# Kernel tuning notes

Hardware: AMD Instinct MI355X
Metric: run time of the kernel (lower is better)

## Reference

```python
import jax, jax.numpy as jnp
import numpy as np

NEG_INF = -1e30  # stand-in for float('-inf') that is fp16/bf16-safe


def setup_inputs() -> dict:
    key = jax.random.key(0)
    ks = jax.random.split(key, 6)
    B, S, D, E = 4, 4096, 2048, 64
    return {
        "x": jax.random.normal(ks[0], (B, S, D), dtype=jnp.float32),
        "router_w": jax.random.normal(ks[1], (E, D), dtype=jnp.float32) * (1.0 / np.sqrt(D)),
        "router_b": jax.random.normal(ks[2], (E,), dtype=jnp.float32) * 0.01,
        "noise_w": jax.random.normal(ks[3], (E, D), dtype=jnp.float32) * (1.0 / np.sqrt(D)),
        "noise_b": jax.random.normal(ks[4], (E,), dtype=jnp.float32) * 0.01,
        "noise_u": jax.random.uniform(ks[5], (B, S, E), dtype=jnp.float32),
        "top_k": 2,
    }


def reference(x, router_w, router_b, noise_w, noise_b, noise_u, top_k):
    E = router_w.shape[0]
    # dual linear projections: [B,S,D] x [D,E] -> [B,S,E]
    logits = jnp.einsum("bsd,ed->bse", x, router_w) + router_b
    noise_scale = jax.nn.softplus(jnp.einsum("bsd,ed->bse", x, noise_w) + noise_b)
    noisy = logits + noise_scale * noise_u  # noise_u plays role of torch.rand_like
    # top-k over experts
    max_k, max_k_index = jax.lax.top_k(noisy, top_k)  # [B,S,k]
    # scatter top-k values into -inf-filled tensor == keep noisy at topk slots
    keep = jnp.sum(jax.nn.one_hot(max_k_index, E, dtype=noisy.dtype), axis=-2) > 0  # [B,S,E]
    sparse = jnp.where(keep, noisy, NEG_INF)
    sf_sparse_topk = jax.nn.softmax(sparse, axis=-1)
    return (sf_sparse_topk, max_k_index)
```

## Files before the change

kernel.cpp:

```cpp
#include <hip/hip_runtime.h>
#include <math.h>

typedef __fp16   fp16x2  __attribute__((ext_vector_type(2)));
typedef _Float16 half8   __attribute__((ext_vector_type(8)));
typedef float    floatx4 __attribute__((ext_vector_type(4)));

#define M_TOTAL 16384
#define K_DIM   2048
#define NCOL    128
#define BM      32
#define BK      32
#define NT      256
#define NCHUNK  (K_DIM / BK)

#define A_HI  0
#define A_LO  1024
#define B_HI  2048
#define B_LO  6144
#define BUF_H 10240

__device__ __forceinline__ void gl_lds16(const _Float16* g, _Float16* l) {
    __builtin_amdgcn_global_load_lds((const __attribute__((address_space(1))) void*)g,
                                     (__attribute__((address_space(3))) void*)l, 16, 0, 0);
}

__device__ __forceinline__ void cvt_store(const float4 v, _Float16* hiP, _Float16* loP) {
    fp16x2 h01 = __builtin_amdgcn_cvt_pkrtz(v.x, v.y);
    fp16x2 h23 = __builtin_amdgcn_cvt_pkrtz(v.z, v.w);
    float r0 = (v.x - (float)h01.x) * 2048.0f;
    float r1 = (v.y - (float)h01.y) * 2048.0f;
    float r2 = (v.z - (float)h23.x) * 2048.0f;
    float r3 = (v.w - (float)h23.y) * 2048.0f;
    fp16x2 l01 = __builtin_amdgcn_cvt_pkrtz(r0, r1);
    fp16x2 l23 = __builtin_amdgcn_cvt_pkrtz(r2, r3);
    union { fp16x2 h[2]; uint2 u; } ph, pl;
    ph.h[0] = h01; ph.h[1] = h23;
    pl.h[0] = l01; pl.h[1] = l23;
    *(uint2*)hiP = ph.u;
    *(uint2*)loP = pl.u;
}

__global__ __launch_bounds__(256) void conv_w_kernel(
    const float* __restrict__ rw, const float* __restrict__ nw,
    _Float16* __restrict__ wsB)
{
    const int u   = blockIdx.x * 256 + threadIdx.x;
    const int col = u & 127;
    const int g   = (u >> 7) & 3;
    const int c   = u >> 9;
    const float* srcRow = (col < 64) ? (rw + (size_t)col * K_DIM)
                                     : (nw + (size_t)(col - 64) * K_DIM);
    const float* src = srcRow + c * BK + g * 8;
    const float4 v0 = *(const float4*)src;
    const float4 v1 = *(const float4*)(src + 4);
    union { fp16x2 h[4]; uint4 q; } ph, pl;
    ph.h[0] = __builtin_amdgcn_cvt_pkrtz(v0.x, v0.y);
    ph.h[1] = __builtin_amdgcn_cvt_pkrtz(v0.z, v0.w);
    ph.h[2] = __builtin_amdgcn_cvt_pkrtz(v1.x, v1.y);
    ph.h[3] = __builtin_amdgcn_cvt_pkrtz(v1.z, v1.w);
    pl.h[0] = __builtin_amdgcn_cvt_pkrtz((v0.x - (float)ph.h[0].x) * 2048.0f,
                                         (v0.y - (float)ph.h[0].y) * 2048.0f);
    pl.h[1] = __builtin_amdgcn_cvt_pkrtz((v0.z - (float)ph.h[1].x) * 2048.0f,
                                         (v0.w - (float)ph.h[1].y) * 2048.0f);
    pl.h[2] = __builtin_amdgcn_cvt_pkrtz((v1.x - (float)ph.h[2].x) * 2048.0f,
                                         (v1.y - (float)ph.h[2].y) * 2048.0f);
    pl.h[3] = __builtin_amdgcn_cvt_pkrtz((v1.z - (float)ph.h[3].x) * 2048.0f,
                                         (v1.w - (float)ph.h[3].y) * 2048.0f);
    const size_t base = (size_t)c * 8192 + ((size_t)g * 128 + col) * 8;
    *(uint4*)&wsB[base]        = ph.q;
    *(uint4*)&wsB[base + 4096] = pl.q;
}

__global__ __launch_bounds__(NT, 2) void gemm_router_kernel(
    const float* __restrict__ x,
    const _Float16* __restrict__ wsB,
    const float* __restrict__ router_b,
    const float* __restrict__ noise_b,
    const float* __restrict__ noise_u,
    float* __restrict__ out)
{
    __shared__ __align__(16) union {
        _Float16 S[2 * BUF_H];
        struct { float Cs[32][132]; float p1[32]; float p2[32]; int i1[32]; int i2[32]; } e;
    } sm;

    const int t    = threadIdx.x;
    const int lane = t & 63;
    const int w    = t >> 6;
    const int rowBase = blockIdx.x * BM;

    const int r = t >> 3, q = t & 7;
    const float* pa = x + (size_t)(rowBase + r) * K_DIM + q * 4;
    const int aw = ((q >> 1) * 32 + r) * 8 + (q & 1) * 4;

    const int lr  = lane & 15;
    const int lg4 = lane >> 4;
    const int mt0 = (w & 1) * 16;
    const int nt0 = (w >> 1) * 64;
    const int aOff = (lg4 * 32 + mt0 + lr) * 8;

    floatx4 acch[4], accx[4];
    #pragma unroll
    for (int ni = 0; ni < 4; ++ni) { acch[ni] = (floatx4)0.0f; accx[ni] = (floatx4)0.0f; }

    float4 aReg = *(const float4*)pa;
    {
        #pragma unroll
        for (int i = 0; i < 4; ++i) {
            const int n = w * 4 + i;
            gl_lds16(wsB + n * 512 + lane * 8, &sm.S[B_HI + n * 512]);
        }
    }
    cvt_store(aReg, &sm.S[A_HI + aw], &sm.S[A_LO + aw]);

    for (int c = 0; c < NCHUNK; ++c) {
        __syncthreads();
        _Float16* buf  = sm.S + (c & 1) * BUF_H;
        _Float16* bufn = sm.S + ((c + 1) & 1) * BUF_H;

        if (c + 1 < NCHUNK) {
            const _Float16* wc = wsB + (size_t)(c + 1) * 8192;
            #pragma unroll
            for (int i = 0; i < 4; ++i) {
                const int n = w * 4 + i;
                gl_lds16(wc + n * 512 + lane * 8, bufn + B_HI + n * 512);
            }
            aReg = *(const float4*)(pa + (c + 1) * BK);
        }

        const half8 ah = *(const half8*)&buf[A_HI + aOff];
        const half8 al = *(const half8*)&buf[A_LO + aOff];
        half8 bh[4], bl[4];
        #pragma unroll
        for (int ni = 0; ni < 4; ++ni) {
            const int bo = (lg4 * 128 + nt0 + ni * 16 + lr) * 8;
            bh[ni] = *(const half8*)&buf[B_HI + bo];
            bl[ni] = *(const half8*)&buf[B_LO + bo];
        }
        #pragma unroll
        for (int ni = 0; ni < 4; ++ni) {
            acch[ni] = __builtin_amdgcn_mfma_f32_16x16x32_f16(ah, bh[ni], acch[ni], 0, 0, 0);
            accx[ni] = __builtin_amdgcn_mfma_f32_16x16x32_f16(ah, bl[ni], accx[ni], 0, 0, 0);
            accx[ni] = __builtin_amdgcn_mfma_f32_16x16x32_f16(al, bh[ni], accx[ni], 0, 0, 0);
        }
        if (c + 1 < NCHUNK)
            cvt_store(aReg, &bufn[A_HI + aw], &bufn[A_LO + aw]);
    }

    #pragma unroll
    for (int ni = 0; ni < 4; ++ni) {
        const floatx4 v = acch[ni] + accx[ni] * (1.0f / 2048.0f);
        const int col = nt0 + ni * 16 + lr;
        #pragma unroll
        for (int reg = 0; reg < 4; ++reg)
            sm.e.Cs[mt0 + lg4 * 4 + reg][col] = v[reg];
    }
    __syncthreads();

    {
        const int sr = t >> 3;
        const int eg = (t & 7) * 8;
        const int grow = rowBase + sr;
        const float* urow = noise_u + (size_t)grow * 64 + eg;
        const float4 u0 = *(const float4*)urow;
        const float4 u1 = *(const float4*)(urow + 4);
        const float uu[8] = {u0.x, u0.y, u0.z, u0.w, u1.x, u1.y, u1.z, u1.w};
        float v1 = -3.0e38f, v2 = -3.0e38f;
        int i1 = 0, i2 = 0;
        #pragma unroll
        for (int j = 0; j < 8; ++j) {
            const int e = eg + j;
            const float lg = sm.e.Cs[sr][e] + router_b[e];
            const float nz = sm.e.Cs[sr][64 + e] + noise_b[e];
            const float sp = fmaxf(nz, 0.0f) + log1pf(expf(-fabsf(nz)));
            const float nv = lg + sp * uu[j];
            if (nv > v1)      { v2 = v1; i2 = i1; v1 = nv; i1 = e; }
            else if (nv > v2) { v2 = nv; i2 = e; }
        }
        #pragma unroll
        for (int m = 1; m < 8; m <<= 1) {
            const float ov1 = __shfl_xor(v1, m, 64);
            const int   oi1 = __shfl_xor(i1, m, 64);
            const float ov2 = __shfl_xor(v2, m, 64);
            const int   oi2 = __shfl_xor(i2, m, 64);
            const bool takeO = (ov1 > v1) || (ov1 == v1 && oi1 < i1);
            const float t1v = takeO ? ov1 : v1;  const int t1i = takeO ? oi1 : i1;
            const float c2v = takeO ? v1 : ov1;  const int c2i = takeO ? i1 : oi1;
            const float c3v = takeO ? ov2 : v2;  const int c3i = takeO ? oi2 : i2;
            const bool k2 = (c3v > c2v) || (c3v == c2v && c3i < c2i);
            v1 = t1v; i1 = t1i;
            v2 = k2 ? c3v : c2v; i2 = k2 ? c3i : c2i;
        }
        if ((t & 7) == 0) {
            const float e2 = expf(v2 - v1);
            const float dn = 1.0f + e2;
            sm.e.p1[sr] = 1.0f / dn;
            sm.e.p2[sr] = e2 / dn;
            sm.e.i1[sr] = i1;
            sm.e.i2[sr] = i2;
            float2 idx2;
            idx2.x = (float)i1;
            idx2.y = (float)i2;
            *(float2*)&out[(size_t)M_TOTAL * 64 + (size_t)grow * 2] = idx2;
        }
    }
    __syncthreads();

    {
        const int rr = t >> 3;
        const int e0 = (t & 7) * 8;
        const int g2 = rowBase + rr;
        const int j1 = sm.e.i1[rr], j2 = sm.e.i2[rr];
        const float q1 = sm.e.p1[rr], q2 = sm.e.p2[rr];
        float* orow = out + (size_t)g2 * 64;
        #pragma unroll
        for (int g = 0; g < 2; ++g) {
            const int b0 = e0 + g * 4;
            float4 v;
            v.x = (b0 + 0 == j1) ? q1 : (b0 + 0 == j2) ? q2 : 0.0f;
            v.y = (b0 + 1 == j1) ? q1 : (b0 + 1 == j2) ? q2 : 0.0f;
            v.z = (b0 + 2 == j1) ? q1 : (b0 + 2 == j2) ? q2 : 0.0f;
            v.w = (b0 + 3 == j1) ? q1 : (b0 + 3 == j2) ? q2 : 0.0f;
            *(float4*)&orow[b0] = v;
        }
    }
}

extern "C" void kernel_launch(void* const* d_in, const int* in_sizes, int n_in,
                              void* d_out, int out_size, void* d_ws, size_t ws_size,
                              hipStream_t stream) {
    const float* x  = (const float*)d_in[0];
    const float* rw = (const float*)d_in[1];
    const float* rb = (const float*)d_in[2];
    const float* nw = (const float*)d_in[3];
    const float* nb = (const float*)d_in[4];
    const float* nu = (const float*)d_in[5];
    float* out = (float*)d_out;
    _Float16* wsB = (_Float16*)d_ws;
    (void)in_sizes; (void)n_in; (void)out_size; (void)ws_size;

    hipLaunchKernelGGL(conv_w_kernel, dim3(128), dim3(256), 0, stream, rw, nw, wsB);
    hipLaunchKernelGGL(gemm_router_kernel, dim3(M_TOTAL / BM), dim3(NT), 0, stream,
                       x, wsB, rb, nb, nu, out);
}
```

Baseline: 239.7 us.

## Load GEMM operands straight into registers and drop LDS staging and barriers

The main loop no longer stages x and the split-fp16 weights through double-buffered LDS with a barrier each chunk. Each wave now loads its own A fragments (fp32, converted to hi/lo fp16 in registers) and B fragments directly from global memory into registers, prefetching one chunk ahead. The per-wave tile changes from 16x64 to 32x32, and the MFMA block is wrapped in s_setprio. This removes LDS traffic and the per-chunk __syncthreads, at the cost of non-coalesced global loads and duplicated A loads and conversions across the four waves, which now all read the same rows.

```diff
diff --git a/kernel.cpp b/kernel.cpp
--- a/kernel.cpp
+++ b/kernel.cpp
@@ -7,38 +7,9 @@
 
 #define M_TOTAL 16384
 #define K_DIM   2048
-#define NCOL    128
 #define BM      32
-#define BK      32
 #define NT      256
-#define NCHUNK  (K_DIM / BK)
-
-#define A_HI  0
-#define A_LO  1024
-#define B_HI  2048
-#define B_LO  6144
-#define BUF_H 10240
-
-__device__ __forceinline__ void gl_lds16(const _Float16* g, _Float16* l) {
-    __builtin_amdgcn_global_load_lds((const __attribute__((address_space(1))) void*)g,
-                                     (__attribute__((address_space(3))) void*)l, 16, 0, 0);
-}
-
-__device__ __forceinline__ void cvt_store(const float4 v, _Float16* hiP, _Float16* loP) {
-    fp16x2 h01 = __builtin_amdgcn_cvt_pkrtz(v.x, v.y);
-    fp16x2 h23 = __builtin_amdgcn_cvt_pkrtz(v.z, v.w);
-    float r0 = (v.x - (float)h01.x) * 2048.0f;
-    float r1 = (v.y - (float)h01.y) * 2048.0f;
-    float r2 = (v.z - (float)h23.x) * 2048.0f;
-    float r3 = (v.w - (float)h23.y) * 2048.0f;
-    fp16x2 l01 = __builtin_amdgcn_cvt_pkrtz(r0, r1);
-    fp16x2 l23 = __builtin_amdgcn_cvt_pkrtz(r2, r3);
-    union { fp16x2 h[2]; uint2 u; } ph, pl;
-    ph.h[0] = h01; ph.h[1] = h23;
-    pl.h[0] = l01; pl.h[1] = l23;
-    *(uint2*)hiP = ph.u;
-    *(uint2*)loP = pl.u;
-}
+#define NCHUNK  64
 
 __global__ __launch_bounds__(256) void conv_w_kernel(
     const float* __restrict__ rw, const float* __restrict__ nw,
@@ -50,7 +21,7 @@
     const int c   = u >> 9;
     const float* srcRow = (col < 64) ? (rw + (size_t)col * K_DIM)
                                      : (nw + (size_t)(col - 64) * K_DIM);
-    const float* src = srcRow + c * BK + g * 8;
+    const float* src = srcRow + c * 32 + g * 8;
     const float4 v0 = *(const float4*)src;
     const float4 v1 = *(const float4*)(src + 4);
     union { fp16x2 h[4]; uint4 q; } ph, pl;
@@ -71,6 +42,24 @@
     *(uint4*)&wsB[base + 4096] = pl.q;
 }
 
+__device__ __forceinline__ void cvt8(const float4 v0, const float4 v1,
+                                     half8& hi, half8& lo) {
+    union { fp16x2 h[4]; half8 v; } H, L;
+    H.h[0] = __builtin_amdgcn_cvt_pkrtz(v0.x, v0.y);
+    H.h[1] = __builtin_amdgcn_cvt_pkrtz(v0.z, v0.w);
+    H.h[2] = __builtin_amdgcn_cvt_pkrtz(v1.x, v1.y);
+    H.h[3] = __builtin_amdgcn_cvt_pkrtz(v1.z, v1.w);
+    L.h[0] = __builtin_amdgcn_cvt_pkrtz((v0.x - (float)H.h[0].x) * 2048.0f,
+                                        (v0.y - (float)H.h[0].y) * 2048.0f);
+    L.h[1] = __builtin_amdgcn_cvt_pkrtz((v0.z - (float)H.h[1].x) * 2048.0f,
+                                        (v0.w - (float)H.h[1].y) * 2048.0f);
+    L.h[2] = __builtin_amdgcn_cvt_pkrtz((v1.x - (float)H.h[2].x) * 2048.0f,
+                                        (v1.y - (float)H.h[2].y) * 2048.0f);
+    L.h[3] = __builtin_amdgcn_cvt_pkrtz((v1.z - (float)H.h[3].x) * 2048.0f,
+                                        (v1.w - (float)H.h[3].y) * 2048.0f);
+    hi = H.v; lo = L.v;
+}
+
 __global__ __launch_bounds__(NT, 2) void gemm_router_kernel(
     const float* __restrict__ x,
     const _Float16* __restrict__ wsB,
@@ -79,82 +68,93 @@
     const float* __restrict__ noise_u,
     float* __restrict__ out)
 {
-    __shared__ __align__(16) union {
-        _Float16 S[2 * BUF_H];
-        struct { float Cs[32][132]; float p1[32]; float p2[32]; int i1[32]; int i2[32]; } e;
-    } sm;
+    __shared__ __align__(16) struct {
+        float Cs[32][132]; float p1[32]; float p2[32]; int i1[32]; int i2[32];
+    } sme;
 
     const int t    = threadIdx.x;
     const int lane = t & 63;
     const int w    = t >> 6;
     const int rowBase = blockIdx.x * BM;
 
-    const int r = t >> 3, q = t & 7;
-    const float* pa = x + (size_t)(rowBase + r) * K_DIM + q * 4;
-    const int aw = ((q >> 1) * 32 + r) * 8 + (q & 1) * 4;
-
     const int lr  = lane & 15;
     const int lg4 = lane >> 4;
-    const int mt0 = (w & 1) * 16;
-    const int nt0 = (w >> 1) * 64;
-    const int aOff = (lg4 * 32 + mt0 + lr) * 8;
-
-    floatx4 acch[4], accx[4];
-    #pragma unroll
-    for (int ni = 0; ni < 4; ++ni) { acch[ni] = (floatx4)0.0f; accx[ni] = (floatx4)0.0f; }
-
-    float4 aReg = *(const float4*)pa;
-    {
-        #pragma unroll
-        for (int i = 0; i < 4; ++i) {
-            const int n = w * 4 + i;
-            gl_lds16(wsB + n * 512 + lane * 8, &sm.S[B_HI + n * 512]);
-        }
-    }
-    cvt_store(aReg, &sm.S[A_HI + aw], &sm.S[A_LO + aw]);
+    const int nt0 = w * 32;
+
+    const float* pax = x + (size_t)(rowBase + lr) * K_DIM + lg4 * 8;
+    const _Float16* pb = wsB + ((size_t)lg4 * 128 + nt0 + lr) * 8;
+
+    floatx4 acch[2][2], accx[2][2];
+    #pragma unroll
+    for (int mi = 0; mi < 2; ++mi)
+        #pragma unroll
+        for (int ni = 0; ni < 2; ++ni) {
+            acch[mi][ni] = (floatx4)0.0f;
+            accx[mi][ni] = (floatx4)0.0f;
+        }
+
+    float4 aCur[4], aNxt[4];
+    half8  bhC[2], blC[2], bhN[2], blN[2];
+
+    #pragma unroll
+    for (int mi = 0; mi < 2; ++mi)
+        #pragma unroll
+        for (int h = 0; h < 2; ++h)
+            aCur[mi * 2 + h] = *(const float4*)(pax + mi * 16 * K_DIM + h * 4);
+    #pragma unroll
+    for (int ni = 0; ni < 2; ++ni) {
+        bhC[ni] = *(const half8*)(pb + ni * 128);
+        blC[ni] = *(const half8*)(pb + ni * 128 + 4096);
+    }
 
     for (int c = 0; c < NCHUNK; ++c) {
-        __syncthreads();
-        _Float16* buf  = sm.S + (c & 1) * BUF_H;
-        _Float16* bufn = sm.S + ((c + 1) & 1) * BUF_H;
-
-        if (c + 1 < NCHUNK) {
-            const _Float16* wc = wsB + (size_t)(c + 1) * 8192;
+        const int cn = (c + 1 < NCHUNK) ? c + 1 : NCHUNK - 1;
+        const float* pan = pax + cn * 32;
+        const _Float16* pbn = pb + (size_t)cn * 8192;
+        #pragma unroll
+        for (int mi = 0; mi < 2; ++mi)
             #pragma unroll
-            for (int i = 0; i < 4; ++i) {
-                const int n = w * 4 + i;
-                gl_lds16(wc + n * 512 + lane * 8, bufn + B_HI + n * 512);
+            for (int h = 0; h < 2; ++h)
+                aNxt[mi * 2 + h] = *(const float4*)(pan + mi * 16 * K_DIM + h * 4);
+        #pragma unroll
+        for (int ni = 0; ni < 2; ++ni) {
+            bhN[ni] = *(const half8*)(pbn + ni * 128);
+            blN[ni] = *(const half8*)(pbn + ni * 128 + 4096);
+        }
+
+        half8 ah[2], al[2];
+        cvt8(aCur[0], aCur[1], ah[0], al[0]);
+        cvt8(aCur[2], aCur[3], ah[1], al[1]);
+
+        __builtin_amdgcn_s_setprio(1);
+        #pragma unroll
+        for (int mi = 0; mi < 2; ++mi)
+            #pragma unroll
+            for (int ni = 0; ni < 2; ++ni) {
+                acch[mi][ni] = __builtin_amdgcn_mfma_f32_16x16x32_f16(ah[mi], bhC[ni], acch[mi][ni], 0, 0, 0);
+                accx[mi][ni] = __builtin_amdgcn_mfma_f32_16x16x32_f16(ah[mi], blC[ni], accx[mi][ni], 0, 0, 0);
+                accx[mi][ni] = __builtin_amdgcn_mfma_f32_16x16x32_f16(al[mi], bhC[ni], accx[mi][ni], 0, 0, 0);
             }
-            aReg = *(const float4*)(pa + (c + 1) * BK);
-        }
-
-        const half8 ah = *(const half8*)&buf[A_HI + aOff];
-        const half8 al = *(const half8*)&buf[A_LO + aOff];
-        half8 bh[4], bl[4];
-        #pragma unroll
-        for (int ni = 0; ni < 4; ++ni) {
-            const int bo = (lg4 * 128 + nt0 + ni * 16 + lr) * 8;
-            bh[ni] = *(const half8*)&buf[B_HI + bo];
-            bl[ni] = *(const half8*)&buf[B_LO + bo];
-        }
-        #pragma unroll
-        for (int ni = 0; ni < 4; ++ni) {
-            acch[ni] = __builtin_amdgcn_mfma_f32_16x16x32_f16(ah, bh[ni], acch[ni], 0, 0, 0);
-            accx[ni] = __builtin_amdgcn_mfma_f32_16x16x32_f16(ah, bl[ni], accx[ni], 0, 0, 0);
-            accx[ni] = __builtin_amdgcn_mfma_f32_16x16x32_f16(al, bh[ni], accx[ni], 0, 0, 0);
-        }
-        if (c + 1 < NCHUNK)
-            cvt_store(aReg, &bufn[A_HI + aw], &bufn[A_LO + aw]);
-    }
-
-    #pragma unroll
-    for (int ni = 0; ni < 4; ++ni) {
-        const floatx4 v = acch[ni] + accx[ni] * (1.0f / 2048.0f);
-        const int col = nt0 + ni * 16 + lr;
-        #pragma unroll
-        for (int reg = 0; reg < 4; ++reg)
-            sm.e.Cs[mt0 + lg4 * 4 + reg][col] = v[reg];
-    }
+        __builtin_amdgcn_s_setprio(0);
+
+        #pragma unroll
+        for (int i = 0; i < 4; ++i) aCur[i] = aNxt[i];
+        #pragma unroll
+        for (int ni = 0; ni < 2; ++ni) {
+            bhC[ni] = bhN[ni]; blC[ni] = blN[ni];
+        }
+    }
+
+    #pragma unroll
+    for (int mi = 0; mi < 2; ++mi)
+        #pragma unroll
+        for (int ni = 0; ni < 2; ++ni) {
+            const floatx4 v = acch[mi][ni] + accx[mi][ni] * (1.0f / 2048.0f);
+            const int col = nt0 + ni * 16 + lr;
+            #pragma unroll
+            for (int reg = 0; reg < 4; ++reg)
+                sme.Cs[mi * 16 + lg4 * 4 + reg][col] = v[reg];
+        }
     __syncthreads();
 
     {
@@ -170,8 +170,8 @@
         #pragma unroll
         for (int j = 0; j < 8; ++j) {
             const int e = eg + j;
-            const float lg = sm.e.Cs[sr][e] + router_b[e];
-            const float nz = sm.e.Cs[sr][64 + e] + noise_b[e];
+            const float lg = sme.Cs[sr][e] + router_b[e];
+            const float nz = sme.Cs[sr][64 + e] + noise_b[e];
             const float sp = fmaxf(nz, 0.0f) + log1pf(expf(-fabsf(nz)));
             const float nv = lg + sp * uu[j];
             if (nv > v1)      { v2 = v1; i2 = i1; v1 = nv; i1 = e; }
@@ -194,10 +194,10 @@
         if ((t & 7) == 0) {
             const float e2 = expf(v2 - v1);
             const float dn = 1.0f + e2;
-            sm.e.p1[sr] = 1.0f / dn;
-            sm.e.p2[sr] = e2 / dn;
-            sm.e.i1[sr] = i1;
-            sm.e.i2[sr] = i2;
+            sme.p1[sr] = 1.0f / dn;
+            sme.p2[sr] = e2 / dn;
+            sme.i1[sr] = i1;
+            sme.i2[sr] = i2;
             float2 idx2;
             idx2.x = (float)i1;
             idx2.y = (float)i2;
@@ -210,8 +210,8 @@
         const int rr = t >> 3;
         const int e0 = (t & 7) * 8;
         const int g2 = rowBase + rr;
-        const int j1 = sm.e.i1[rr], j2 = sm.e.i2[rr];
-        const float q1 = sm.e.p1[rr], q2 = sm.e.p2[rr];
+        const int j1 = sme.i1[rr], j2 = sme.i2[rr];
+        const float q1 = sme.p1[rr], q2 = sme.p2[rr];
         float* orow = out + (size_t)g2 * 64;
         #pragma unroll
         for (int g = 0; g < 2; ++g) {
```

After: 249.5 us. 1.04x slower.

## Enlarge row tile to 64 with 512 threads and 2x2 MFMA warp tiles

Applied to the files above, without the earlier changes.

Doubles the block's row tile from 32 to 64 and the thread count from 256 to 512. The 128 output columns are now split across four column groups of warps, and each warp computes a 2x2 grid of 16x16 MFMA tiles. Each B chunk of weights loaded into LDS is therefore reused across twice as many rows, which halves weight traffic per row and the number of blocks. The LDS buffers and epilogue arrays grow to match, and a sync is added before the epilogue writes, since the Cs area overlaps the staging buffers. The trade-off is fewer blocks (256 on a GPU with many CUs) and possibly lower occupancy.

```diff
diff --git a/kernel.cpp b/kernel.cpp
--- a/kernel.cpp
+++ b/kernel.cpp
@@ -7,17 +7,16 @@
 
 #define M_TOTAL 16384
 #define K_DIM   2048
-#define NCOL    128
-#define BM      32
+#define BM      64
 #define BK      32
-#define NT      256
+#define NT      512
 #define NCHUNK  (K_DIM / BK)
 
 #define A_HI  0
-#define A_LO  1024
-#define B_HI  2048
-#define B_LO  6144
-#define BUF_H 10240
+#define A_LO  2048
+#define B_HI  4096
+#define B_LO  8192
+#define BUF_H 12288
 
 __device__ __forceinline__ void gl_lds16(const _Float16* g, _Float16* l) {
     __builtin_amdgcn_global_load_lds((const __attribute__((address_space(1))) void*)g,
@@ -81,7 +80,7 @@
 {
     __shared__ __align__(16) union {
         _Float16 S[2 * BUF_H];
-        struct { float Cs[32][132]; float p1[32]; float p2[32]; int i1[32]; int i2[32]; } e;
+        struct { float Cs[64][132]; float p1[64]; float p2[64]; int i1[64]; int i2[64]; } e;
     } sm;
 
     const int t    = threadIdx.x;
@@ -91,70 +90,90 @@
 
     const int r = t >> 3, q = t & 7;
     const float* pa = x + (size_t)(rowBase + r) * K_DIM + q * 4;
-    const int aw = ((q >> 1) * 32 + r) * 8 + (q & 1) * 4;
+    const int aw = ((q >> 1) * 64 + r) * 8 + (q & 1) * 4;
 
     const int lr  = lane & 15;
     const int lg4 = lane >> 4;
-    const int mt0 = (w & 1) * 16;
-    const int nt0 = (w >> 1) * 64;
-    const int aOff = (lg4 * 32 + mt0 + lr) * 8;
-
-    floatx4 acch[4], accx[4];
+    const int wr  = w & 1;
+    const int wc  = w >> 1;
+    const int mt0 = wr * 32;
+    const int nt0 = wc * 32;
+
+    floatx4 acch[2][2], accx[2][2];
     #pragma unroll
-    for (int ni = 0; ni < 4; ++ni) { acch[ni] = (floatx4)0.0f; accx[ni] = (floatx4)0.0f; }
-
-    float4 aReg = *(const float4*)pa;
-    {
-        #pragma unroll
-        for (int i = 0; i < 4; ++i) {
-            const int n = w * 4 + i;
+    for (int mi = 0; mi < 2; ++mi)
+        #pragma unroll
+        for (int ni = 0; ni < 2; ++ni) {
+            acch[mi][ni] = (floatx4)0.0f;
+            accx[mi][ni] = (floatx4)0.0f;
+        }
+
+    {
+        #pragma unroll
+        for (int i = 0; i < 2; ++i) {
+            const int n = w * 2 + i;
             gl_lds16(wsB + n * 512 + lane * 8, &sm.S[B_HI + n * 512]);
         }
     }
-    cvt_store(aReg, &sm.S[A_HI + aw], &sm.S[A_LO + aw]);
+    {
+        const float4 a0 = *(const float4*)pa;
+        cvt_store(a0, &sm.S[A_HI + aw], &sm.S[A_LO + aw]);
+    }
 
     for (int c = 0; c < NCHUNK; ++c) {
         __syncthreads();
         _Float16* buf  = sm.S + (c & 1) * BUF_H;
         _Float16* bufn = sm.S + ((c + 1) & 1) * BUF_H;
 
+        float4 aReg;
         if (c + 1 < NCHUNK) {
-            const _Float16* wc = wsB + (size_t)(c + 1) * 8192;
+            const _Float16* wcp = wsB + (size_t)(c + 1) * 8192;
             #pragma unroll
-            for (int i = 0; i < 4; ++i) {
-                const int n = w * 4 + i;
-                gl_lds16(wc + n * 512 + lane * 8, bufn + B_HI + n * 512);
+            for (int i = 0; i < 2; ++i) {
+                const int n = w * 2 + i;
+                gl_lds16(wcp + n * 512 + lane * 8, bufn + B_HI + n * 512);
             }
             aReg = *(const float4*)(pa + (c + 1) * BK);
         }
 
-        const half8 ah = *(const half8*)&buf[A_HI + aOff];
-        const half8 al = *(const half8*)&buf[A_LO + aOff];
-        half8 bh[4], bl[4];
-        #pragma unroll
-        for (int ni = 0; ni < 4; ++ni) {
+        half8 ah[2], al[2];
+        #pragma unroll
+        for (int mi = 0; mi < 2; ++mi) {
+            const int ao = (lg4 * 64 + mt0 + mi * 16 + lr) * 8;
+            ah[mi] = *(const half8*)&buf[A_HI + ao];
+            al[mi] = *(const half8*)&buf[A_LO + ao];
+        }
+        half8 bh[2], bl[2];
+        #pragma unroll
+        for (int ni = 0; ni < 2; ++ni) {
             const int bo = (lg4 * 128 + nt0 + ni * 16 + lr) * 8;
             bh[ni] = *(const half8*)&buf[B_HI + bo];
             bl[ni] = *(const half8*)&buf[B_LO + bo];
         }
         #pragma unroll
-        for (int ni = 0; ni < 4; ++ni) {
-            acch[ni] = __builtin_amdgcn_mfma_f32_16x16x32_f16(ah, bh[ni], acch[ni], 0, 0, 0);
-            accx[ni] = __builtin_amdgcn_mfma_f32_16x16x32_f16(ah, bl[ni], accx[ni], 0, 0, 0);
-            accx[ni] = __builtin_amdgcn_mfma_f32_16x16x32_f16(al, bh[ni], accx[ni], 0, 0, 0);
-        }
+        for (int mi = 0; mi < 2; ++mi)
+            #pragma unroll
+            for (int ni = 0; ni < 2; ++ni) {
+                acch[mi][ni] = __builtin_amdgcn_mfma_f32_16x16x32_f16(ah[mi], bh[ni], acch[mi][ni], 0, 0, 0);
+                accx[mi][ni] = __builtin_amdgcn_mfma_f32_16x16x32_f16(ah[mi], bl[ni], accx[mi][ni], 0, 0, 0);
+                accx[mi][ni] = __builtin_amdgcn_mfma_f32_16x16x32_f16(al[mi], bh[ni], accx[mi][ni], 0, 0, 0);
+            }
         if (c + 1 < NCHUNK)
             cvt_store(aReg, &bufn[A_HI + aw], &bufn[A_LO + aw]);
     }
 
+    __syncthreads();
+
     #pragma unroll
-    for (int ni = 0; ni < 4; ++ni) {
-        const floatx4 v = acch[ni] + accx[ni] * (1.0f / 2048.0f);
-        const int col = nt0 + ni * 16 + lr;
-        #pragma unroll
-        for (int reg = 0; reg < 4; ++reg)
-            sm.e.Cs[mt0 + lg4 * 4 + reg][col] = v[reg];
-    }
+    for (int mi = 0; mi < 2; ++mi)
+        #pragma unroll
+        for (int ni = 0; ni < 2; ++ni) {
+            const floatx4 v = acch[mi][ni] + accx[mi][ni] * (1.0f / 2048.0f);
+            const int col = nt0 + ni * 16 + lr;
+            #pragma unroll
+            for (int reg = 0; reg < 4; ++reg)
+                sm.e.Cs[mt0 + mi * 16 + lg4 * 4 + reg][col] = v[reg];
+        }
     __syncthreads();
 
     {
```

Measured after the change: 236.3 us. No clear change (-1.4%).

## Split GEMM along K into two partial kernels plus separate router epilogue

Applied to the files above, without the earlier changes.

Splits the K dimension in half so 1024 blocks each compute a partial 32x128 product, which doubles the grid and raises the occupancy hint to 4. The partials are written to workspace and summed in a new epilogue kernel that does bias, softplus, top-2 and softmax. The aim is more parallelism and latency hiding on a grid that was only 512 blocks. The cost is a round trip of the partials through global memory and an extra launch. The fused path is kept as a fallback when the workspace is too small.

```diff
diff --git a/kernel.cpp b/kernel.cpp
--- a/kernel.cpp
+++ b/kernel.cpp
@@ -7,17 +7,21 @@
 
 #define M_TOTAL 16384
 #define K_DIM   2048
-#define NCOL    128
 #define BM      32
 #define BK      32
 #define NT      256
 #define NCHUNK  (K_DIM / BK)
+#define NCH_H   32
 
 #define A_HI  0
 #define A_LO  1024
 #define B_HI  2048
 #define B_LO  6144
 #define BUF_H 10240
+
+#define WS_B_BYTES   (1u << 20)
+#define WS_PART_F    ((size_t)M_TOTAL * 128)
+#define WS_NEED      (WS_B_BYTES + 2 * WS_PART_F * sizeof(float) + 65536)
 
 __device__ __forceinline__ void gl_lds16(const _Float16* g, _Float16* l) {
     __builtin_amdgcn_global_load_lds((const __attribute__((address_space(1))) void*)g,
@@ -71,26 +75,22 @@
     *(uint4*)&wsB[base + 4096] = pl.q;
 }
 
-__global__ __launch_bounds__(NT, 2) void gemm_router_kernel(
+__global__ __launch_bounds__(NT, 4) void gemm_partial_kernel(
     const float* __restrict__ x,
     const _Float16* __restrict__ wsB,
-    const float* __restrict__ router_b,
-    const float* __restrict__ noise_b,
-    const float* __restrict__ noise_u,
-    float* __restrict__ out)
+    float* __restrict__ part)
 {
-    __shared__ __align__(16) union {
-        _Float16 S[2 * BUF_H];
-        struct { float Cs[32][132]; float p1[32]; float p2[32]; int i1[32]; int i2[32]; } e;
-    } sm;
+    __shared__ __align__(16) _Float16 S[2 * BUF_H];
 
     const int t    = threadIdx.x;
     const int lane = t & 63;
     const int w    = t >> 6;
-    const int rowBase = blockIdx.x * BM;
+    const int tile = blockIdx.x & 511;
+    const int kh   = blockIdx.x >> 9;
+    const int rowBase = tile * BM;
 
     const int r = t >> 3, q = t & 7;
-    const float* pa = x + (size_t)(rowBase + r) * K_DIM + q * 4;
+    const float* pa = x + (size_t)(rowBase + r) * K_DIM + kh * (NCH_H * BK) + q * 4;
     const int aw = ((q >> 1) * 32 + r) * 8 + (q & 1) * 4;
 
     const int lr  = lane & 15;
@@ -99,27 +99,32 @@
     const int nt0 = (w >> 1) * 64;
     const int aOff = (lg4 * 32 + mt0 + lr) * 8;
 
+    const _Float16* wsBase = wsB + (size_t)kh * NCH_H * 8192;
+
     floatx4 acch[4], accx[4];
     #pragma unroll
     for (int ni = 0; ni < 4; ++ni) { acch[ni] = (floatx4)0.0f; accx[ni] = (floatx4)0.0f; }
 
-    float4 aReg = *(const float4*)pa;
     {
         #pragma unroll
         for (int i = 0; i < 4; ++i) {
             const int n = w * 4 + i;
-            gl_lds16(wsB + n * 512 + lane * 8, &sm.S[B_HI + n * 512]);
-        }
-    }
-    cvt_store(aReg, &sm.S[A_HI + aw], &sm.S[A_LO + aw]);
-
-    for (int c = 0; c < NCHUNK; ++c) {
+            gl_lds16(wsBase + n * 512 + lane * 8, &S[B_HI + n * 512]);
+        }
+    }
+    {
+        const float4 a0 = *(const float4*)pa;
+        cvt_store(a0, &S[A_HI + aw], &S[A_LO + aw]);
+    }
+
+    for (int c = 0; c < NCH_H; ++c) {
         __syncthreads();
-        _Float16* buf  = sm.S + (c & 1) * BUF_H;
-        _Float16* bufn = sm.S + ((c + 1) & 1) * BUF_H;
-
-        if (c + 1 < NCHUNK) {
-            const _Float16* wc = wsB + (size_t)(c + 1) * 8192;
+        _Float16* buf  = S + (c & 1) * BUF_H;
+        _Float16* bufn = S + ((c + 1) & 1) * BUF_H;
+
+        float4 aReg;
+        if (c + 1 < NCH_H) {
+            const _Float16* wc = wsBase + (size_t)(c + 1) * 8192;
             #pragma unroll
             for (int i = 0; i < 4; ++i) {
                 const int n = w * 4 + i;
@@ -143,37 +148,72 @@
             accx[ni] = __builtin_amdgcn_mfma_f32_16x16x32_f16(ah, bl[ni], accx[ni], 0, 0, 0);
             accx[ni] = __builtin_amdgcn_mfma_f32_16x16x32_f16(al, bh[ni], accx[ni], 0, 0, 0);
         }
-        if (c + 1 < NCHUNK)
+        if (c + 1 < NCH_H)
             cvt_store(aReg, &bufn[A_HI + aw], &bufn[A_LO + aw]);
     }
 
+    float* myP = part + (size_t)kh * WS_PART_F + (size_t)rowBase * 128;
     #pragma unroll
     for (int ni = 0; ni < 4; ++ni) {
         const floatx4 v = acch[ni] + accx[ni] * (1.0f / 2048.0f);
         const int col = nt0 + ni * 16 + lr;
         #pragma unroll
         for (int reg = 0; reg < 4; ++reg)
-            sm.e.Cs[mt0 + lg4 * 4 + reg][col] = v[reg];
-    }
-    __syncthreads();
-
-    {
-        const int sr = t >> 3;
-        const int eg = (t & 7) * 8;
-        const int grow = rowBase + sr;
+            myP[(size_t)(mt0 + lg4 * 4 + reg) * 128 + col] = v[reg];
+    }
+}
+
+__global__ __launch_bounds__(256) void router_epilogue_kernel(
+    const float* __restrict__ part,
+    const float* __restrict__ router_b,
+    const float* __restrict__ noise_b,
+    const float* __restrict__ noise_u,
+    float* __restrict__ out)
+{
+    __shared__ struct { float p1[32]; float p2[32]; int i1[32]; int i2[32]; } sm;
+
+    const int t  = threadIdx.x;
+    const int sr = t >> 3;
+    const int tg = t & 7;
+    const int eg = tg * 8;
+    const int grow = blockIdx.x * 32 + sr;
+
+    {
+        const float* q0 = part + (size_t)grow * 128;
+        const float* q1 = part + WS_PART_F + (size_t)grow * 128;
+        const float4 l0a = *(const float4*)(q0 + eg);
+        const float4 l0b = *(const float4*)(q0 + eg + 4);
+        const float4 l1a = *(const float4*)(q1 + eg);
+        const float4 l1b = *(const float4*)(q1 + eg + 4);
+        const float4 n0a = *(const float4*)(q0 + 64 + eg);
+        const float4 n0b = *(const float4*)(q0 + 64 + eg + 4);
+        const float4 n1a = *(const float4*)(q1 + 64 + eg);
+        const float4 n1b = *(const float4*)(q1 + 64 + eg + 4);
+        const float4 rba = *(const float4*)(router_b + eg);
+        const float4 rbb = *(const float4*)(router_b + eg + 4);
+        const float4 nba = *(const float4*)(noise_b + eg);
+        const float4 nbb = *(const float4*)(noise_b + eg + 4);
         const float* urow = noise_u + (size_t)grow * 64 + eg;
         const float4 u0 = *(const float4*)urow;
         const float4 u1 = *(const float4*)(urow + 4);
+
+        const float lg_[8] = {l0a.x + l1a.x + rba.x, l0a.y + l1a.y + rba.y,
+                              l0a.z + l1a.z + rba.z, l0a.w + l1a.w + rba.w,
+                              l0b.x + l1b.x + rbb.x, l0b.y + l1b.y + rbb.y,
+                              l0b.z + l1b.z + rbb.z, l0b.w + l1b.w + rbb.w};
+        const float nz_[8] = {n0a.x + n1a.x + nba.x, n0a.y + n1a.y + nba.y,
+                              n0a.z + n1a.z + nba.z, n0a.w + n1a.w + nba.w,
+                              n0b.x + n1b.x + nbb.x, n0b.y + n1b.y + nbb.y,
+                              n0b.z + n1b.z + nbb.z, n0b.w + n1b.w + nbb.w};
         const float uu[8] = {u0.x, u0.y, u0.z, u0.w, u1.x, u1.y, u1.z, u1.w};
+
         float v1 = -3.0e38f, v2 = -3.0e38f;
         int i1 = 0, i2 = 0;
         #pragma unroll
         for (int j = 0; j < 8; ++j) {
             const int e = eg + j;
-            const float lg = sm.e.Cs[sr][e] + router_b[e];
-            const float nz = sm.e.Cs[sr][64 + e] + noise_b[e];
-            const float sp = fmaxf(nz, 0.0f) + log1pf(expf(-fabsf(nz)));
-            const float nv = lg + sp * uu[j];
+            const float sp = fmaxf(nz_[j], 0.0f) + log1pf(expf(-fabsf(nz_[j])));
+            const float nv = lg_[j] + sp * uu[j];
             if (nv > v1)      { v2 = v1; i2 = i1; v1 = nv; i1 = e; }
             else if (nv > v2) { v2 = nv; i2 = e; }
         }
@@ -191,6 +231,164 @@
             v1 = t1v; i1 = t1i;
             v2 = k2 ? c3v : c2v; i2 = k2 ? c3i : c2i;
         }
+        if (tg == 0) {
+            const float e2 = expf(v2 - v1);
+            const float dn = 1.0f + e2;
+            sm.p1[sr] = 1.0f / dn;
+            sm.p2[sr] = e2 / dn;
+            sm.i1[sr] = i1;
+            sm.i2[sr] = i2;
+            float2 idx2;
+            idx2.x = (float)i1;
+            idx2.y = (float)i2;
+            *(float2*)&out[(size_t)M_TOTAL * 64 + (size_t)grow * 2] = idx2;
+        }
+    }
+    __syncthreads();
+
+    {
+        const int rr = t >> 3;
+        const int e0 = (t & 7) * 8;
+        const int g2 = blockIdx.x * 32 + rr;
+        const int j1 = sm.i1[rr], j2 = sm.i2[rr];
+        const float q1 = sm.p1[rr], q2 = sm.p2[rr];
+        float* orow = out + (size_t)g2 * 64;
+        #pragma unroll
+        for (int g = 0; g < 2; ++g) {
+            const int b0 = e0 + g * 4;
+            float4 v;
+            v.x = (b0 + 0 == j1) ? q1 : (b0 + 0 == j2) ? q2 : 0.0f;
+            v.y = (b0 + 1 == j1) ? q1 : (b0 + 1 == j2) ? q2 : 0.0f;
+            v.z = (b0 + 2 == j1) ? q1 : (b0 + 2 == j2) ? q2 : 0.0f;
+            v.w = (b0 + 3 == j1) ? q1 : (b0 + 3 == j2) ? q2 : 0.0f;
+            *(float4*)&orow[b0] = v;
+        }
+    }
+}
+
+__global__ __launch_bounds__(NT, 2) void gemm_router_fused(
+    const float* __restrict__ x,
+    const _Float16* __restrict__ wsB,
+    const float* __restrict__ router_b,
+    const float* __restrict__ noise_b,
+    const float* __restrict__ noise_u,
+    float* __restrict__ out)
+{
+    __shared__ __align__(16) union {
+        _Float16 S[2 * BUF_H];
+        struct { float Cs[32][132]; float p1[32]; float p2[32]; int i1[32]; int i2[32]; } e;
+    } sm;
+
+    const int t    = threadIdx.x;
+    const int lane = t & 63;
+    const int w    = t >> 6;
+    const int rowBase = blockIdx.x * BM;
+
+    const int r = t >> 3, q = t & 7;
+    const float* pa = x + (size_t)(rowBase + r) * K_DIM + q * 4;
+    const int aw = ((q >> 1) * 32 + r) * 8 + (q & 1) * 4;
+
+    const int lr  = lane & 15;
+    const int lg4 = lane >> 4;
+    const int mt0 = (w & 1) * 16;
+    const int nt0 = (w >> 1) * 64;
+    const int aOff = (lg4 * 32 + mt0 + lr) * 8;
+
+    floatx4 acch[4], accx[4];
+    #pragma unroll
+    for (int ni = 0; ni < 4; ++ni) { acch[ni] = (floatx4)0.0f; accx[ni] = (floatx4)0.0f; }
+
+    {
+        #pragma unroll
+        for (int i = 0; i < 4; ++i) {
+            const int n = w * 4 + i;
+            gl_lds16(wsB + n * 512 + lane * 8, &sm.S[B_HI + n * 512]);
+        }
+    }
+    {
+        const float4 a0 = *(const float4*)pa;
+        cvt_store(a0, &sm.S[A_HI + aw], &sm.S[A_LO + aw]);
+    }
+
+    for (int c = 0; c < NCHUNK; ++c) {
+        __syncthreads();
+        _Float16* buf  = sm.S + (c & 1) * BUF_H;
+        _Float16* bufn = sm.S + ((c + 1) & 1) * BUF_H;
+
+        float4 aReg;
+        if (c + 1 < NCHUNK) {
+            const _Float16* wc = wsB + (size_t)(c + 1) * 8192;
+            #pragma unroll
+            for (int i = 0; i < 4; ++i) {
+                const int n = w * 4 + i;
+                gl_lds16(wc + n * 512 + lane * 8, bufn + B_HI + n * 512);
+            }
+            aReg = *(const float4*)(pa + (c + 1) * BK);
+        }
+
+        const half8 ah = *(const half8*)&buf[A_HI + aOff];
+        const half8 al = *(const half8*)&buf[A_LO + aOff];
+        half8 bh[4], bl[4];
+        #pragma unroll
+        for (int ni = 0; ni < 4; ++ni) {
+            const int bo = (lg4 * 128 + nt0 + ni * 16 + lr) * 8;
+            bh[ni] = *(const half8*)&buf[B_HI + bo];
+            bl[ni] = *(const half8*)&buf[B_LO + bo];
+        }
+        #pragma unroll
+        for (int ni = 0; ni < 4; ++ni) {
+            acch[ni] = __builtin_amdgcn_mfma_f32_16x16x32_f16(ah, bh[ni], acch[ni], 0, 0, 0);
+            accx[ni] = __builtin_amdgcn_mfma_f32_16x16x32_f16(ah, bl[ni], accx[ni], 0, 0, 0);
+            accx[ni] = __builtin_amdgcn_mfma_f32_16x16x32_f16(al, bh[ni], accx[ni], 0, 0, 0);
+        }
+        if (c + 1 < NCHUNK)
+            cvt_store(aReg, &bufn[A_HI + aw], &bufn[A_LO + aw]);
+    }
+
+    #pragma unroll
+    for (int ni = 0; ni < 4; ++ni) {
+        const floatx4 v = acch[ni] + accx[ni] * (1.0f / 2048.0f);
+        const int col = nt0 + ni * 16 + lr;
+        #pragma unroll
+        for (int reg = 0; reg < 4; ++reg)
+            sm.e.Cs[mt0 + lg4 * 4 + reg][col] = v[reg];
+    }
+    __syncthreads();
+
+    {
+        const int sr = t >> 3;
+        const int eg = (t & 7) * 8;
+        const int grow = rowBase + sr;
+        const float* urow = noise_u + (size_t)grow * 64 + eg;
+        const float4 u0 = *(const float4*)urow;
+        const float4 u1 = *(const float4*)(urow + 4);
+        const float uu[8] = {u0.x, u0.y, u0.z, u0.w, u1.x, u1.y, u1.z, u1.w};
+        float v1 = -3.0e38f, v2 = -3.0e38f;
+        int i1 = 0, i2 = 0;
+        #pragma unroll
+        for (int j = 0; j < 8; ++j) {
+            const int e = eg + j;
+            const float lg = sm.e.Cs[sr][e] + router_b[e];
+            const float nz = sm.e.Cs[sr][64 + e] + noise_b[e];
+            const float sp = fmaxf(nz, 0.0f) + log1pf(expf(-fabsf(nz)));
+            const float nv = lg + sp * uu[j];
+            if (nv > v1)      { v2 = v1; i2 = i1; v1 = nv; i1 = e; }
+            else if (nv > v2) { v2 = nv; i2 = e; }
+        }
+        #pragma unroll
+        for (int m = 1; m < 8; m <<= 1) {
+            const float ov1 = __shfl_xor(v1, m, 64);
+            const int   oi1 = __shfl_xor(i1, m, 64);
+            const float ov2 = __shfl_xor(v2, m, 64);
+            const int   oi2 = __shfl_xor(i2, m, 64);
+            const bool takeO = (ov1 > v1) || (ov1 == v1 && oi1 < i1);
+            const float t1v = takeO ? ov1 : v1;  const int t1i = takeO ? oi1 : i1;
+            const float c2v = takeO ? v1 : ov1;  const int c2i = takeO ? i1 : oi1;
+            const float c3v = takeO ? ov2 : v2;  const int c3i = takeO ? oi2 : i2;
+            const bool k2 = (c3v > c2v) || (c3v == c2v && c3i < c2i);
+            v1 = t1v; i1 = t1i;
+            v2 = k2 ? c3v : c2v; i2 = k2 ? c3i : c2i;
+        }
         if ((t & 7) == 0) {
             const float e2 = expf(v2 - v1);
             const float dn = 1.0f + e2;
@@ -237,9 +435,18 @@
     const float* nu = (const float*)d_in[5];
     float* out = (float*)d_out;
     _Float16* wsB = (_Float16*)d_ws;
-    (void)in_sizes; (void)n_in; (void)out_size; (void)ws_size;
+    (void)in_sizes; (void)n_in; (void)out_size;
 
     hipLaunchKernelGGL(conv_w_kernel, dim3(128), dim3(256), 0, stream, rw, nw, wsB);
-    hipLaunchKernelGGL(gemm_router_kernel, dim3(M_TOTAL / BM), dim3(NT), 0, stream,
-                       x, wsB, rb, nb, nu, out);
-}
+
+    if (ws_size >= WS_NEED) {
+        float* part = (float*)((char*)d_ws + WS_B_BYTES);
+        hipLaunchKernelGGL(gemm_partial_kernel, dim3(1024), dim3(NT), 0, stream,
+                           x, wsB, part);
+        hipLaunchKernelGGL(router_epilogue_kernel, dim3(512), dim3(256), 0, stream,
+                           part, rb, nb, nu, out);
+    } else {
+        hipLaunchKernelGGL(gemm_router_fused, dim3(M_TOTAL / BM), dim3(NT), 0, stream,
+                           x, wsB, rb, nb, nu, out);
+    }
+}
```

New measurement: 232.3 us. -3.1%, faster.
